# Kernel optimization log

Hardware: AMD Instinct MI355X
Metric: run time of the kernel (lower is better)

Reference implementation:

```python
import jax, jax.numpy as jnp
import numpy as np

DIM = 512
NUM_HEADS = 8


def setup_inputs() -> dict:
    key = jax.random.key(0)
    ks = jax.random.split(key, 10)
    B, N, C = 2, 4096, DIM
    s = 0.02
    return {
        "x": jax.random.normal(ks[0], (B, N, C), dtype=jnp.float32),
        "Wq": jax.random.normal(ks[1], (C, C), dtype=jnp.float32) * s,
        "Wk": jax.random.normal(ks[2], (C, C), dtype=jnp.float32) * s,
        "Wv": jax.random.normal(ks[3], (C, C), dtype=jnp.float32) * s,
        "Wattn": jax.random.normal(ks[4], (C, C), dtype=jnp.float32) * s,
        "Wconv": jax.random.normal(ks[5], (C, C), dtype=jnp.float32) * s,
        "dw_kernel": jax.random.normal(ks[6], (C, 1, 3), dtype=jnp.float32) * s,  # depthwise (O, I/groups, K)
        "dw_bias": jax.random.normal(ks[7], (C,), dtype=jnp.float32) * s,
        "Wcout": jax.random.normal(ks[8], (C, C), dtype=jnp.float32) * s,
        "H": 8,
        "W": 512,
    }


def reference(x, Wq, Wk, Wv, Wattn, Wconv, dw_kernel, dw_bias, Wcout, H, W):
    B, N, C = x.shape
    nh = NUM_HEADS
    hd = C // nh
    scale = hd ** (-0.5)

    # QKV projections (torch Linear: x @ W.T), split heads -> [B, nh, N, hd]
    q = (x @ Wq.T).reshape(B, N, nh, hd).transpose(0, 2, 1, 3)
    k = (x @ Wk.T).reshape(B, N, nh, hd).transpose(0, 2, 1, 3)
    v = (x @ Wv.T).reshape(B, N, nh, hd).transpose(0, 2, 1, 3)

    # Materialized N x N attention (faithful to source)
    scores = jnp.einsum("bhqd,bhkd->bhqk", q, k) * scale
    weights = jax.nn.softmax(scores, axis=-1)
    attn = jnp.einsum("bhqk,bhkd->bhqd", weights, v)
    attn = attn.transpose(0, 2, 1, 3).reshape(B, N, C)
    attn_out = attn @ Wattn.T

    # Parallel depthwise-conv branch
    ci = (x @ Wconv.T).transpose(0, 2, 1)  # [B, C, N]
    co = jax.lax.conv_general_dilated(
        ci, dw_kernel,
        window_strides=(1,), padding=((1, 1),),
        feature_group_count=C,
        dimension_numbers=("NCH", "OIH", "NCH"),
    ) + dw_bias[None, :, None]
    conv_out = co.transpose(0, 2, 1) @ Wcout.T  # [B, N, C]

    out = attn_out + conv_out
    # NOTE: source shadows arg H with num_heads before the view
    return out.reshape(B, nh, W, C)
```

## Files before the change

### kernel.cpp

```cpp
#include <hip/hip_runtime.h>

typedef __attribute__((ext_vector_type(8))) short bf16x8;
typedef __attribute__((ext_vector_type(4))) float f32x4;

constexpr int kB = 2, kN = 4096, kC = 512, kNH = 8, kHD = 64;
constexpr int kBN = kB * kN;
constexpr int kWElems = 262144;
constexpr int kWAll = 6 * kWElems;
constexpr int kWExtra = 3584;
constexpr float kQScale = 0.1803368801f;

__device__ __forceinline__ short f2bf(float f) {
  union { float f; unsigned u; } v; v.f = f;
  unsigned r = v.u + 0x7fffu + ((v.u >> 16) & 1u);
  return (short)(r >> 16);
}
__device__ __forceinline__ float bf2f(short s) {
  union { unsigned u; float f; } v; v.u = ((unsigned)(unsigned short)s) << 16;
  return v.f;
}
__device__ __forceinline__ float exp2_(float x) {
#if __has_builtin(__builtin_amdgcn_exp2f)
  return __builtin_amdgcn_exp2f(x);
#else
  return exp2f(x);
#endif
}
__device__ __forceinline__ unsigned pk2bf(float a, float b) {
  union { float f; unsigned u; } ua, ub; ua.f = a; ub.f = b;
#if __has_builtin(__builtin_amdgcn_perm)
  return __builtin_amdgcn_perm(ub.u + 0x8000u, ua.u + 0x8000u, 0x07060302u);
#else
  return ((ua.u + 0x8000u) >> 16) | (((ub.u + 0x8000u) >> 16) << 16);
#endif
}

__device__ __forceinline__ bf16x8 ld8(const short* p) { return *(const bf16x8*)p; }
__device__ __forceinline__ bf16x8 ld8(const float* p) {
  float4 a = *(const float4*)p;
  float4 b = *(const float4*)(p + 4);
  bf16x8 r;
  r[0] = f2bf(a.x); r[1] = f2bf(a.y); r[2] = f2bf(a.z); r[3] = f2bf(a.w);
  r[4] = f2bf(b.x); r[5] = f2bf(b.y); r[6] = f2bf(b.z); r[7] = f2bf(b.w);
  return r;
}
__device__ __forceinline__ void stf(short* p, float v) { *p = f2bf(v); }
__device__ __forceinline__ void stf(float* p, float v) { *p = v; }

__device__ __forceinline__ void gload_lds16(const void* g, void* l) {
  __builtin_amdgcn_global_load_lds(
      (const __attribute__((address_space(1))) void*)g,
      (__attribute__((address_space(3))) void*)l, 16, 0, 0);
}

__global__ void detect_dtype(const unsigned* __restrict__ x, int* __restrict__ flag) {
  const int lane = threadIdx.x & 63;
  unsigned w = x[lane];
  int e = (int)((w >> 7) & 0xffu);
  bool bf = (e >= 100 && e <= 140);
  unsigned long long m = __ballot(bf);
  if (lane == 0) *flag = (__popcll(m) >= 32) ? 1 : 0;
}

constexpr int kW8 = kWAll / 8;
constexpr int kX8 = kBN * kC / 8;
__global__ __launch_bounds__(256) void convert_all(
    const void* Wq, const void* Wk, const void* Wv, const void* Wc,
    const void* Wa, const void* Wco, const void* dwk, const void* dwb,
    const void* x, const int* __restrict__ flag, short* __restrict__ dst,
    short* __restrict__ xb) {
  const int gtid = blockIdx.x * 256 + threadIdx.x;
  const bool bf = (*flag != 0);
  if (gtid < kW8) {
    const int e = gtid * 8;
    const int t = e >> 18, off = e & (kWElems - 1);
    const void* src = (t == 0) ? Wq : (t == 1) ? Wk : (t == 2) ? Wv
                    : (t == 3) ? Wc : (t == 4) ? Wa : Wco;
    bf16x8 v = bf ? ld8((const short*)src + off) : ld8((const float*)src + off);
    *(bf16x8*)(dst + e) = v;
  } else if (gtid < kW8 + kWExtra) {
    const int eoff = gtid - kW8;
    if (eoff < 1536) {
      dst[kWAll + eoff] = bf ? ((const short*)dwk)[eoff]
                             : f2bf(((const float*)dwk)[eoff]);
    } else if (eoff < 2048) {
      const int i = eoff - 1536;
      dst[kWAll + 1536 + i] = bf ? ((const short*)dwb)[i]
                                 : f2bf(((const float*)dwb)[i]);
    } else {
      const int t2 = eoff - 2048;
      const int tap = t2 >> 9, c = t2 & 511;
      dst[kWAll + 2048 + t2] = bf ? ((const short*)dwk)[c * 3 + tap]
                                  : f2bf(((const float*)dwk)[c * 3 + tap]);
    }
  } else if (gtid < kW8 + kWExtra + kX8) {
    const int e = (gtid - kW8 - kWExtra) * 8;
    bf16x8 v = bf ? ld8((const short*)x + e) : ld8((const float*)x + e);
    *(bf16x8*)(xb + e) = v;
  }
}

__global__ __launch_bounds__(256, 3) void proj_gemm(
    const short* __restrict__ xb, const short* __restrict__ wb,
    short* __restrict__ q, short* __restrict__ k, short* __restrict__ vT,
    short* __restrict__ ci) {
  __shared__ __align__(16) short As[128 * 64];
  __shared__ __align__(16) short Bs[128 * 64];
  const int t = threadIdx.x;
  const int wave = t >> 6, lane = t & 63;
  const int row = lane & 15, quad = lane >> 4;
  const int bn = blockIdx.x & 15;
  const int bm = blockIdx.x >> 4;
  const int m0 = bm * 128, n0 = bn * 128;
  const int wm = wave & 1, wn = wave >> 1;
  const int lrow = lane >> 3, lch = lane & 7;

  f32x4 acc[4][4];
#pragma unroll
  for (int mi = 0; mi < 4; ++mi)
#pragma unroll
    for (int ni = 0; ni < 4; ++ni)
#pragma unroll
      for (int r = 0; r < 4; ++r) acc[mi][ni][r] = 0.0f;

  for (int k0 = 0; k0 < kC; k0 += 64) {
#pragma unroll
    for (int p = 0; p < 4; ++p) {
      const int m = wave * 32 + p * 8 + lrow;
      const int kch = lch ^ (m & 7);
      gload_lds16(xb + (size_t)(m0 + m) * kC + k0 + kch * 8,
                  &As[(wave * 32 + p * 8) * 64]);
      gload_lds16(wb + (size_t)(n0 + m) * kC + k0 + kch * 8,
                  &Bs[(wave * 32 + p * 8) * 64]);
    }
    __syncthreads();

#pragma unroll
    for (int kk2 = 0; kk2 < 2; ++kk2) {
      bf16x8 af[4], bfr[4];
#pragma unroll
      for (int mi = 0; mi < 4; ++mi) {
        const int m = wm * 64 + mi * 16 + row;
        const int ch = (kk2 * 4 + quad) ^ (m & 7);
        af[mi] = *(const bf16x8*)(&As[m * 64 + ch * 8]);
      }
#pragma unroll
      for (int ni = 0; ni < 4; ++ni) {
        const int n = wn * 64 + ni * 16 + row;
        const int ch = (kk2 * 4 + quad) ^ (n & 7);
        bfr[ni] = *(const bf16x8*)(&Bs[n * 64 + ch * 8]);
      }
#pragma unroll
      for (int mi = 0; mi < 4; ++mi)
#pragma unroll
        for (int ni = 0; ni < 4; ++ni)
          acc[mi][ni] = __builtin_amdgcn_mfma_f32_16x16x32_bf16(
              af[mi], bfr[ni], acc[mi][ni], 0, 0, 0);
    }
    __syncthreads();
  }

  const int gc0 = n0 + wn * 64;
  const int mat = gc0 >> 9;
  const float scale = (mat == 0) ? kQScale : 1.0f;
#pragma unroll
  for (int mi = 0; mi < 4; ++mi) {
#pragma unroll
    for (int ni = 0; ni < 4; ++ni) {
#pragma unroll
      for (int r = 0; r < 4; ++r) {
        const int gm = m0 + wm * 64 + mi * 16 + quad * 4 + r;
        const int c_ = ((gc0 + ni * 16) & 511) + row;
        const int b_ = gm >> 12;
        const int n_ = gm & (kN - 1);
        const short bv = f2bf(acc[mi][ni][r] * scale);
        if (mat == 3) {
          ci[(b_ * kN + n_) * kC + c_] = bv;
        } else {
          const int h = c_ >> 6, d = c_ & 63;
          const int bh = b_ * kNH + h;
          if (mat == 0)      q[(bh * kN + n_) * kHD + d] = bv;
          else if (mat == 1) k[(bh * kN + n_) * kHD + d] = bv;
          else               vT[(bh * kHD + d) * kN + n_] = bv;
        }
      }
    }
  }
}

__global__ __launch_bounds__(256) void dwconv(
    const short* __restrict__ ci, const short* __restrict__ wb,
    short* __restrict__ cb) {
  const int e0 = (blockIdx.x * 256 + threadIdx.x) * 8;
  const int c0 = e0 & (kC - 1);
  const int bn = e0 >> 9;
  const int n_ = bn & (kN - 1);
  bf16x8 xc = ld8(ci + e0);
  bf16x8 xm, xp;
  if (n_ > 0) xm = ld8(ci + e0 - kC);
  else
#pragma unroll
    for (int i = 0; i < 8; ++i) xm[i] = 0;
  if (n_ < kN - 1) xp = ld8(ci + e0 + kC);
  else
#pragma unroll
    for (int i = 0; i < 8; ++i) xp[i] = 0;
  bf16x8 w0 = ld8(wb + kWAll + 2048 + c0);
  bf16x8 w1 = ld8(wb + kWAll + 2048 + 512 + c0);
  bf16x8 w2 = ld8(wb + kWAll + 2048 + 1024 + c0);
  bf16x8 bi = ld8(wb + kWAll + 1536 + c0);
  bf16x8 o;
#pragma unroll
  for (int i = 0; i < 8; ++i) {
    float a = bf2f(bi[i]) + bf2f(xm[i]) * bf2f(w0[i]) +
              bf2f(xc[i]) * bf2f(w1[i]) + bf2f(xp[i]) * bf2f(w2[i]);
    o[i] = f2bf(a);
  }
  *(bf16x8*)(cb + e0) = o;
}

__global__ __launch_bounds__(256, 3) void attn_flash(
    const short* __restrict__ q, const short* __restrict__ k,
    const short* __restrict__ vT, short* __restrict__ attn) {
  __shared__ __align__(16) short Kb[2][64 * 72];
  __shared__ __align__(16) short VbS[2][64 * 72];
  const int t = threadIdx.x;
  const int wave = t >> 6;
  const int lane = t & 63;
  const int row = lane & 15;
  const int quad = lane >> 4;

  const int slot = blockIdx.x & 7;
  const int inner = blockIdx.x >> 3;
  const int bh = slot * 2 + (inner & 1);
  const int q0 = (inner >> 1) * 128 + wave * 32;

  const short* qbase = q + (bh * kN + q0) * kHD;
  const short* kbase = k + bh * kN * kHD;
  const short* vbase = vT + bh * kHD * kN;

  bf16x8 qb[2][2];
#pragma unroll
  for (int g = 0; g < 2; ++g) {
    qb[g][0] = *(const bf16x8*)(qbase + (g * 16 + row) * kHD + quad * 8);
    qb[g][1] = *(const bf16x8*)(qbase + (g * 16 + row) * kHD + 32 + quad * 8);
  }

  f32x4 o[2][4];
#pragma unroll
  for (int g = 0; g < 2; ++g)
#pragma unroll
    for (int j = 0; j < 4; ++j)
#pragma unroll
      for (int r = 0; r < 4; ++r) o[g][j][r] = 0.0f;
  float l_[2] = {0.0f, 0.0f};

  const int i0 = t, i1 = t + 256;
  const int sr0 = i0 >> 3, sc0 = i0 & 7;
  const int sr1 = i1 >> 3, sc1 = i1 & 7;
  const int vb0 = (sc0 >> 2) * 32 + (sc0 & 1) * 16 + (sc0 & 2) * 2;
  const int vb1 = (sc1 >> 2) * 32 + (sc1 & 1) * 16 + (sc1 & 2) * 2;

  auto stage_v = [&](int buf, bf16x8 v0, bf16x8 v1) {
    *(short4*)(&VbS[buf][sr0 * 72 + vb0]) =
        make_short4(v0[0], v0[1], v0[2], v0[3]);
    *(short4*)(&VbS[buf][sr0 * 72 + vb0 + 8]) =
        make_short4(v0[4], v0[5], v0[6], v0[7]);
    *(short4*)(&VbS[buf][sr1 * 72 + vb1]) =
        make_short4(v1[0], v1[1], v1[2], v1[3]);
    *(short4*)(&VbS[buf][sr1 * 72 + vb1 + 8]) =
        make_short4(v1[4], v1[5], v1[6], v1[7]);
  };

  {
    bf16x8 ka = *(const bf16x8*)(kbase + i0 * 8);
    bf16x8 kb2 = *(const bf16x8*)(kbase + i1 * 8);
    *(bf16x8*)(&Kb[0][sr0 * 72 + sc0 * 8]) = ka;
    *(bf16x8*)(&Kb[0][sr1 * 72 + sc1 * 8]) = kb2;
    bf16x8 v0 = *(const bf16x8*)(vbase + sr0 * kN + sc0 * 8);
    bf16x8 v1 = *(const bf16x8*)(vbase + sr1 * kN + sc1 * 8);
    stage_v(0, v0, v1);
  }
  __syncthreads();

  for (int kt = 0; kt < kN / 64; ++kt) {
    const int cur = kt & 1;
    const bool more = (kt < kN / 64 - 1);
    bf16x8 kn0, kn1, vn0, vn1;
    if (more) {
      kn0 = *(const bf16x8*)(kbase + (kt + 1) * 4096 + i0 * 8);
      kn1 = *(const bf16x8*)(kbase + (kt + 1) * 4096 + i1 * 8);
      vn0 = *(const bf16x8*)(vbase + sr0 * kN + (kt + 1) * 64 + sc0 * 8);
      vn1 = *(const bf16x8*)(vbase + sr1 * kN + (kt + 1) * 64 + sc1 * 8);
    }

    f32x4 s[2][4];
#pragma unroll
    for (int g = 0; g < 2; ++g)
#pragma unroll
      for (int jk = 0; jk < 4; ++jk)
#pragma unroll
        for (int r = 0; r < 4; ++r) s[g][jk][r] = 0.0f;
#pragma unroll
    for (int jk = 0; jk < 4; ++jk) {
      const short* kr = &Kb[cur][(jk * 16 + row) * 72 + quad * 8];
      bf16x8 a0 = *(const bf16x8*)kr;
      bf16x8 a1 = *(const bf16x8*)(kr + 32);
#pragma unroll
      for (int g = 0; g < 2; ++g) {
        s[g][jk] = __builtin_amdgcn_mfma_f32_16x16x32_bf16(a0, qb[g][0], s[g][jk], 0, 0, 0);
        s[g][jk] = __builtin_amdgcn_mfma_f32_16x16x32_bf16(a1, qb[g][1], s[g][jk], 0, 0, 0);
      }
    }

    bf16x8 pb[2][2];
#pragma unroll
    for (int g = 0; g < 2; ++g) {
      float rs = 0.0f;
#pragma unroll
      for (int jk = 0; jk < 4; ++jk)
#pragma unroll
        for (int r = 0; r < 4; ++r) {
          float p = exp2_(s[g][jk][r]);
          s[g][jk][r] = p;
          rs += p;
        }
      l_[g] += rs;
#pragma unroll
      for (int c = 0; c < 2; ++c) {
        union { unsigned u[4]; bf16x8 v; } pu;
        pu.u[0] = pk2bf(s[g][2 * c][0], s[g][2 * c][1]);
        pu.u[1] = pk2bf(s[g][2 * c][2], s[g][2 * c][3]);
        pu.u[2] = pk2bf(s[g][2 * c + 1][0], s[g][2 * c + 1][1]);
        pu.u[3] = pk2bf(s[g][2 * c + 1][2], s[g][2 * c + 1][3]);
        pb[g][c] = pu.v;
      }
    }

#pragma unroll
    for (int jd = 0; jd < 4; ++jd) {
      const short* vb = &VbS[cur][(jd * 16 + row) * 72 + quad * 8];
#pragma unroll
      for (int c = 0; c < 2; ++c) {
        bf16x8 av = *(const bf16x8*)(vb + c * 32);
#pragma unroll
        for (int g = 0; g < 2; ++g)
          o[g][jd] = __builtin_amdgcn_mfma_f32_16x16x32_bf16(
              av, pb[g][c], o[g][jd], 0, 0, 0);
      }
    }

    if (more) {
      *(bf16x8*)(&Kb[1 - cur][sr0 * 72 + sc0 * 8]) = kn0;
      *(bf16x8*)(&Kb[1 - cur][sr1 * 72 + sc1 * 8]) = kn1;
      stage_v(1 - cur, vn0, vn1);
    }
    __syncthreads();
  }

  const int b_ = bh >> 3, h = bh & 7;
#pragma unroll
  for (int g = 0; g < 2; ++g) {
    float lt = l_[g];
    lt += __shfl_xor(lt, 16);
    lt += __shfl_xor(lt, 32);
    const float linv = 1.0f / lt;
    const int n_ = q0 + g * 16 + row;
    short* ob = attn + (b_ * kN + n_) * kC + h * kHD + quad * 4;
#pragma unroll
    for (int jd = 0; jd < 4; ++jd) {
      short4 st = make_short4(f2bf(o[g][jd][0] * linv), f2bf(o[g][jd][1] * linv),
                              f2bf(o[g][jd][2] * linv), f2bf(o[g][jd][3] * linv));
      *(short4*)(ob + jd * 16) = st;
    }
  }
}

template <typename TO>
__device__ __forceinline__ void out_body(
    const short* __restrict__ attn, const short* __restrict__ cb,
    const short* __restrict__ wb, TO* __restrict__ out) {
  __shared__ __align__(16) short As[128 * 64];
  __shared__ __align__(16) short Bs[64 * 64];
  const int t = threadIdx.x;
  const int wave = t >> 6, lane = t & 63;
  const int row = lane & 15, quad = lane >> 4;
  const int bn = blockIdx.x & 7;
  const int bm = blockIdx.x >> 3;
  const int m0 = bm * 128, n0 = bn * 64;
  const int wm = wave & 1, wn = wave >> 1;
  const int lrow = lane >> 3, lch = lane & 7;

  f32x4 acc[4][2];
#pragma unroll
  for (int mi = 0; mi < 4; ++mi)
#pragma unroll
    for (int ni = 0; ni < 2; ++ni)
#pragma unroll
      for (int r = 0; r < 4; ++r) acc[mi][ni][r] = 0.0f;

  const short* Wa = wb + 4 * kWElems;
  const short* Wo = wb + 5 * kWElems;

  for (int k0 = 0; k0 < 1024; k0 += 64) {
    const short* Asrc = (k0 < 512) ? attn : cb;
    const short* Bsrc = (k0 < 512) ? Wa : Wo;
    const int ka = k0 & 511;
#pragma unroll
    for (int p = 0; p < 4; ++p) {
      const int m = wave * 32 + p * 8 + lrow;
      const int kch = lch ^ (m & 7);
      gload_lds16(Asrc + (size_t)(m0 + m) * kC + ka + kch * 8,
                  &As[(wave * 32 + p * 8) * 64]);
    }
#pragma unroll
    for (int p = 0; p < 2; ++p) {
      const int n = wave * 16 + p * 8 + lrow;
      const int kch = lch ^ (n & 7);
      gload_lds16(Bsrc + (size_t)(n0 + n) * kC + ka + kch * 8,
                  &Bs[(wave * 16 + p * 8) * 64]);
    }
    __syncthreads();

#pragma unroll
    for (int kk2 = 0; kk2 < 2; ++kk2) {
      bf16x8 af[4], bfr[2];
#pragma unroll
      for (int mi = 0; mi < 4; ++mi) {
        const int m = wm * 64 + mi * 16 + row;
        const int ch = (kk2 * 4 + quad) ^ (m & 7);
        af[mi] = *(const bf16x8*)(&As[m * 64 + ch * 8]);
      }
#pragma unroll
      for (int ni = 0; ni < 2; ++ni) {
        const int n = wn * 32 + ni * 16 + row;
        const int ch = (kk2 * 4 + quad) ^ (n & 7);
        bfr[ni] = *(const bf16x8*)(&Bs[n * 64 + ch * 8]);
      }
#pragma unroll
      for (int mi = 0; mi < 4; ++mi)
#pragma unroll
        for (int ni = 0; ni < 2; ++ni)
          acc[mi][ni] = __builtin_amdgcn_mfma_f32_16x16x32_bf16(
              af[mi], bfr[ni], acc[mi][ni], 0, 0, 0);
    }
    __syncthreads();
  }

#pragma unroll
  for (int mi = 0; mi < 4; ++mi)
#pragma unroll
    for (int ni = 0; ni < 2; ++ni)
#pragma unroll
      for (int r = 0; r < 4; ++r) {
        const int gm = m0 + wm * 64 + mi * 16 + quad * 4 + r;
        const int gc = n0 + wn * 32 + ni * 16 + row;
        stf(out + (size_t)gm * kC + gc, acc[mi][ni][r]);
      }
}

__global__ __launch_bounds__(256, 4) void out_gemm(
    const short* __restrict__ attn, const short* __restrict__ cb,
    const short* __restrict__ wb, const int* __restrict__ flag, void* out) {
  if (*flag)
    out_body<short>(attn, cb, wb, (short*)out);
  else
    out_body<float>(attn, cb, wb, (float*)out);
}

extern "C" void kernel_launch(void* const* d_in, const int* in_sizes, int n_in,
                              void* d_out, int out_size, void* d_ws, size_t ws_size,
                              hipStream_t stream) {
  const void* x   = d_in[0];
  const void* Wq  = d_in[1];
  const void* Wk  = d_in[2];
  const void* Wv  = d_in[3];
  const void* Wa  = d_in[4];
  const void* Wc  = d_in[5];
  const void* dwk = d_in[6];
  const void* dwb = d_in[7];
  const void* Wco = d_in[8];

  short* ws = (short*)d_ws;
  const size_t E = (size_t)kBN * kC;
  int*   flag = (int*)ws;
  short* wb   = ws + 256;
  short* q    = wb + kWAll + kWExtra;
  short* k    = q + E;
  short* vT   = k + E;
  short* ci   = vT + E;
  short* cb   = ci + E;
  short* attn = ci;
  short* xb   = cb;

  detect_dtype<<<1, 64, 0, stream>>>((const unsigned*)x, flag);
  const int cvt_threads = kW8 + kWExtra + kX8;
  convert_all<<<(cvt_threads + 255) / 256, 256, 0, stream>>>(
      Wq, Wk, Wv, Wc, Wa, Wco, dwk, dwb, x, flag, wb, xb);
  proj_gemm<<<1024, 256, 0, stream>>>(xb, wb, q, k, vT, ci);
  dwconv<<<(kBN * kC) / (256 * 8), 256, 0, stream>>>(ci, wb, cb);
  attn_flash<<<512, 256, 0, stream>>>(q, k, vT, attn);
  out_gemm<<<512, 256, 0, stream>>>(attn, cb, wb, flag, d_out);
}
```

Measured before the change: 246.0 us.

## Halve attention query tile per block and double grid for occupancy

Each wave in the flash attention kernel now processes 16 query rows instead of 32, so a block covers 64 queries and the grid doubles to 1024 blocks. Launch bounds move from 3 to 4 blocks per SIMD budget. This cuts register pressure and raises the number of resident waves to hide latency. The cost is half the reuse of each staged K/V tile, which doubles K/V global and LDS traffic per query.

```diff
diff --git a/kernel.cpp b/kernel.cpp
--- a/kernel.cpp
+++ b/kernel.cpp
@@ -219,7 +219,7 @@
   *(bf16x8*)(cb + e0) = o;
 }
 
-__global__ __launch_bounds__(256, 3) void attn_flash(
+__global__ __launch_bounds__(256, 4) void attn_flash(
     const short* __restrict__ q, const short* __restrict__ k,
     const short* __restrict__ vT, short* __restrict__ attn) {
   __shared__ __align__(16) short Kb[2][64 * 72];
@@ -233,27 +233,22 @@
   const int slot = blockIdx.x & 7;
   const int inner = blockIdx.x >> 3;
   const int bh = slot * 2 + (inner & 1);
-  const int q0 = (inner >> 1) * 128 + wave * 32;
-
-  const short* qbase = q + (bh * kN + q0) * kHD;
-  const short* kbase = k + bh * kN * kHD;
-  const short* vbase = vT + bh * kHD * kN;
-
-  bf16x8 qb[2][2];
-#pragma unroll
-  for (int g = 0; g < 2; ++g) {
-    qb[g][0] = *(const bf16x8*)(qbase + (g * 16 + row) * kHD + quad * 8);
-    qb[g][1] = *(const bf16x8*)(qbase + (g * 16 + row) * kHD + 32 + quad * 8);
-  }
-
-  f32x4 o[2][4];
-#pragma unroll
-  for (int g = 0; g < 2; ++g)
-#pragma unroll
-    for (int j = 0; j < 4; ++j)
-#pragma unroll
-      for (int r = 0; r < 4; ++r) o[g][j][r] = 0.0f;
-  float l_[2] = {0.0f, 0.0f};
+  const int q0 = (inner >> 1) * 64 + wave * 16;
+
+  const short* qbase = q + (size_t)(bh * kN + q0) * kHD;
+  const short* kbase = k + (size_t)bh * kN * kHD;
+  const short* vbase = vT + (size_t)bh * kHD * kN;
+
+  bf16x8 qb[2];
+  qb[0] = *(const bf16x8*)(qbase + row * kHD + quad * 8);
+  qb[1] = *(const bf16x8*)(qbase + row * kHD + 32 + quad * 8);
+
+  f32x4 o[4];
+#pragma unroll
+  for (int jd = 0; jd < 4; ++jd)
+#pragma unroll
+    for (int r = 0; r < 4; ++r) o[jd][r] = 0.0f;
+  float l_ = 0.0f;
 
   const int i0 = t, i1 = t + 256;
   const int sr0 = i0 >> 3, sc0 = i0 & 7;
@@ -294,47 +289,39 @@
       vn1 = *(const bf16x8*)(vbase + sr1 * kN + (kt + 1) * 64 + sc1 * 8);
     }
 
-    f32x4 s[2][4];
-#pragma unroll
-    for (int g = 0; g < 2; ++g)
-#pragma unroll
-      for (int jk = 0; jk < 4; ++jk)
-#pragma unroll
-        for (int r = 0; r < 4; ++r) s[g][jk][r] = 0.0f;
+    f32x4 s[4];
+#pragma unroll
+    for (int jk = 0; jk < 4; ++jk)
+#pragma unroll
+      for (int r = 0; r < 4; ++r) s[jk][r] = 0.0f;
 #pragma unroll
     for (int jk = 0; jk < 4; ++jk) {
       const short* kr = &Kb[cur][(jk * 16 + row) * 72 + quad * 8];
       bf16x8 a0 = *(const bf16x8*)kr;
       bf16x8 a1 = *(const bf16x8*)(kr + 32);
-#pragma unroll
-      for (int g = 0; g < 2; ++g) {
-        s[g][jk] = __builtin_amdgcn_mfma_f32_16x16x32_bf16(a0, qb[g][0], s[g][jk], 0, 0, 0);
-        s[g][jk] = __builtin_amdgcn_mfma_f32_16x16x32_bf16(a1, qb[g][1], s[g][jk], 0, 0, 0);
-      }
-    }
-
-    bf16x8 pb[2][2];
-#pragma unroll
-    for (int g = 0; g < 2; ++g) {
-      float rs = 0.0f;
-#pragma unroll
-      for (int jk = 0; jk < 4; ++jk)
-#pragma unroll
-        for (int r = 0; r < 4; ++r) {
-          float p = exp2_(s[g][jk][r]);
-          s[g][jk][r] = p;
-          rs += p;
-        }
-      l_[g] += rs;
-#pragma unroll
-      for (int c = 0; c < 2; ++c) {
-        union { unsigned u[4]; bf16x8 v; } pu;
-        pu.u[0] = pk2bf(s[g][2 * c][0], s[g][2 * c][1]);
-        pu.u[1] = pk2bf(s[g][2 * c][2], s[g][2 * c][3]);
-        pu.u[2] = pk2bf(s[g][2 * c + 1][0], s[g][2 * c + 1][1]);
-        pu.u[3] = pk2bf(s[g][2 * c + 1][2], s[g][2 * c + 1][3]);
-        pb[g][c] = pu.v;
-      }
+      s[jk] = __builtin_amdgcn_mfma_f32_16x16x32_bf16(a0, qb[0], s[jk], 0, 0, 0);
+      s[jk] = __builtin_amdgcn_mfma_f32_16x16x32_bf16(a1, qb[1], s[jk], 0, 0, 0);
+    }
+
+    float rs = 0.0f;
+#pragma unroll
+    for (int jk = 0; jk < 4; ++jk)
+#pragma unroll
+      for (int r = 0; r < 4; ++r) {
+        float p = exp2_(s[jk][r]);
+        s[jk][r] = p;
+        rs += p;
+      }
+    l_ += rs;
+    bf16x8 pb[2];
+#pragma unroll
+    for (int c = 0; c < 2; ++c) {
+      union { unsigned u[4]; bf16x8 v; } pu;
+      pu.u[0] = pk2bf(s[2 * c][0], s[2 * c][1]);
+      pu.u[1] = pk2bf(s[2 * c][2], s[2 * c][3]);
+      pu.u[2] = pk2bf(s[2 * c + 1][0], s[2 * c + 1][1]);
+      pu.u[3] = pk2bf(s[2 * c + 1][2], s[2 * c + 1][3]);
+      pb[c] = pu.v;
     }
 
 #pragma unroll
@@ -343,10 +330,7 @@
 #pragma unroll
       for (int c = 0; c < 2; ++c) {
         bf16x8 av = *(const bf16x8*)(vb + c * 32);
-#pragma unroll
-        for (int g = 0; g < 2; ++g)
-          o[g][jd] = __builtin_amdgcn_mfma_f32_16x16x32_bf16(
-              av, pb[g][c], o[g][jd], 0, 0, 0);
+        o[jd] = __builtin_amdgcn_mfma_f32_16x16x32_bf16(av, pb[c], o[jd], 0, 0, 0);
       }
     }
 
@@ -359,20 +343,17 @@
   }
 
   const int b_ = bh >> 3, h = bh & 7;
-#pragma unroll
-  for (int g = 0; g < 2; ++g) {
-    float lt = l_[g];
-    lt += __shfl_xor(lt, 16);
-    lt += __shfl_xor(lt, 32);
-    const float linv = 1.0f / lt;
-    const int n_ = q0 + g * 16 + row;
-    short* ob = attn + (b_ * kN + n_) * kC + h * kHD + quad * 4;
-#pragma unroll
-    for (int jd = 0; jd < 4; ++jd) {
-      short4 st = make_short4(f2bf(o[g][jd][0] * linv), f2bf(o[g][jd][1] * linv),
-                              f2bf(o[g][jd][2] * linv), f2bf(o[g][jd][3] * linv));
-      *(short4*)(ob + jd * 16) = st;
-    }
+  float lt = l_;
+  lt += __shfl_xor(lt, 16);
+  lt += __shfl_xor(lt, 32);
+  const float linv = 1.0f / lt;
+  const int n_ = q0 + row;
+  short* ob = attn + (size_t)(b_ * kN + n_) * kC + h * kHD + quad * 4;
+#pragma unroll
+  for (int jd = 0; jd < 4; ++jd) {
+    short4 st = make_short4(f2bf(o[jd][0] * linv), f2bf(o[jd][1] * linv),
+                            f2bf(o[jd][2] * linv), f2bf(o[jd][3] * linv));
+    *(short4*)(ob + jd * 16) = st;
   }
 }
 
@@ -499,6 +480,6 @@
       Wq, Wk, Wv, Wc, Wa, Wco, dwk, dwb, x, flag, wb, xb);
   proj_gemm<<<1024, 256, 0, stream>>>(xb, wb, q, k, vT, ci);
   dwconv<<<(kBN * kC) / (256 * 8), 256, 0, stream>>>(ci, wb, cb);
-  attn_flash<<<512, 256, 0, stream>>>(q, k, vT, attn);
+  attn_flash<<<1024, 256, 0, stream>>>(q, k, vT, attn);
   out_gemm<<<512, 256, 0, stream>>>(attn, cb, wb, flag, d_out);
 }
```

Measured after the change: 275.3 us. 1.12x slower.

## Restructure flash attention K/V pipeline with direct-to-LDS swizzled loads and two-tile phases

Applied to the files above, without the earlier changes.

The attention kernel now processes two 64-key tiles per barrier phase. K is loaded straight into LDS through gload_lds16 into an XOR-swizzled unpadded layout, and V for the next phase is staged between the two tile computations. The aim is to halve the number of barriers and overlap global loads with MFMA work, with s_setprio raised around the MFMA sections. In exchange, LDS use doubles and launch bounds drop from 3 to 2 blocks per CU, which lowers occupancy.

```diff
diff --git a/kernel.cpp b/kernel.cpp
--- a/kernel.cpp
+++ b/kernel.cpp
@@ -219,11 +219,11 @@
   *(bf16x8*)(cb + e0) = o;
 }
 
-__global__ __launch_bounds__(256, 3) void attn_flash(
+__global__ __launch_bounds__(256, 2) void attn_flash(
     const short* __restrict__ q, const short* __restrict__ k,
     const short* __restrict__ vT, short* __restrict__ attn) {
-  __shared__ __align__(16) short Kb[2][64 * 72];
-  __shared__ __align__(16) short VbS[2][64 * 72];
+  __shared__ __align__(16) short Kb[2][2][64 * 64];
+  __shared__ __align__(16) short VbS[2][2][64 * 72];
   const int t = threadIdx.x;
   const int wave = t >> 6;
   const int lane = t & 63;
@@ -235,9 +235,9 @@
   const int bh = slot * 2 + (inner & 1);
   const int q0 = (inner >> 1) * 128 + wave * 32;
 
-  const short* qbase = q + (bh * kN + q0) * kHD;
-  const short* kbase = k + bh * kN * kHD;
-  const short* vbase = vT + bh * kHD * kN;
+  const short* qbase = q + (size_t)(bh * kN + q0) * kHD;
+  const short* kbase = k + (size_t)bh * kN * kHD;
+  const short* vbase = vT + (size_t)bh * kHD * kN;
 
   bf16x8 qb[2][2];
 #pragma unroll
@@ -254,6 +254,9 @@
 #pragma unroll
       for (int r = 0; r < 4; ++r) o[g][j][r] = 0.0f;
   float l_[2] = {0.0f, 0.0f};
+
+  const int ksrow = lane >> 3;
+  const int kschunk = (lane & 7) ^ ksrow;
 
   const int i0 = t, i1 = t + 256;
   const int sr0 = i0 >> 3, sc0 = i0 & 7;
@@ -261,39 +264,31 @@
   const int vb0 = (sc0 >> 2) * 32 + (sc0 & 1) * 16 + (sc0 & 2) * 2;
   const int vb1 = (sc1 >> 2) * 32 + (sc1 & 1) * 16 + (sc1 & 2) * 2;
 
-  auto stage_v = [&](int buf, bf16x8 v0, bf16x8 v1) {
-    *(short4*)(&VbS[buf][sr0 * 72 + vb0]) =
+  auto stage_v = [&](int ph, int tl, bf16x8 v0, bf16x8 v1) {
+    *(short4*)(&VbS[ph][tl][sr0 * 72 + vb0]) =
         make_short4(v0[0], v0[1], v0[2], v0[3]);
-    *(short4*)(&VbS[buf][sr0 * 72 + vb0 + 8]) =
+    *(short4*)(&VbS[ph][tl][sr0 * 72 + vb0 + 8]) =
         make_short4(v0[4], v0[5], v0[6], v0[7]);
-    *(short4*)(&VbS[buf][sr1 * 72 + vb1]) =
+    *(short4*)(&VbS[ph][tl][sr1 * 72 + vb1]) =
         make_short4(v1[0], v1[1], v1[2], v1[3]);
-    *(short4*)(&VbS[buf][sr1 * 72 + vb1 + 8]) =
+    *(short4*)(&VbS[ph][tl][sr1 * 72 + vb1 + 8]) =
         make_short4(v1[4], v1[5], v1[6], v1[7]);
   };
-
-  {
-    bf16x8 ka = *(const bf16x8*)(kbase + i0 * 8);
-    bf16x8 kb2 = *(const bf16x8*)(kbase + i1 * 8);
-    *(bf16x8*)(&Kb[0][sr0 * 72 + sc0 * 8]) = ka;
-    *(bf16x8*)(&Kb[0][sr1 * 72 + sc1 * 8]) = kb2;
-    bf16x8 v0 = *(const bf16x8*)(vbase + sr0 * kN + sc0 * 8);
-    bf16x8 v1 = *(const bf16x8*)(vbase + sr1 * kN + sc1 * 8);
-    stage_v(0, v0, v1);
-  }
-  __syncthreads();
-
-  for (int kt = 0; kt < kN / 64; ++kt) {
-    const int cur = kt & 1;
-    const bool more = (kt < kN / 64 - 1);
-    bf16x8 kn0, kn1, vn0, vn1;
-    if (more) {
-      kn0 = *(const bf16x8*)(kbase + (kt + 1) * 4096 + i0 * 8);
-      kn1 = *(const bf16x8*)(kbase + (kt + 1) * 4096 + i1 * 8);
-      vn0 = *(const bf16x8*)(vbase + sr0 * kN + (kt + 1) * 64 + sc0 * 8);
-      vn1 = *(const bf16x8*)(vbase + sr1 * kN + (kt + 1) * 64 + sc1 * 8);
-    }
-
+  auto stage_k = [&](int ph, int kt2) {
+#pragma unroll
+    for (int tl = 0; tl < 2; ++tl)
+#pragma unroll
+      for (int j = 0; j < 2; ++j)
+        gload_lds16(
+            kbase + (size_t)((kt2 + tl) * 64 + j * 32 + wave * 8 + ksrow) * 64 +
+                kschunk * 8,
+            &Kb[ph][tl][j * 2048 + wave * 512]);
+  };
+
+  const int c0s = ((quad) ^ (row & 7)) * 8;
+  const int c1s = ((quad + 4) ^ (row & 7)) * 8;
+
+  auto tile_step = [&](const short* kt_base, const short* vt_base) {
     f32x4 s[2][4];
 #pragma unroll
     for (int g = 0; g < 2; ++g)
@@ -301,31 +296,31 @@
       for (int jk = 0; jk < 4; ++jk)
 #pragma unroll
         for (int r = 0; r < 4; ++r) s[g][jk][r] = 0.0f;
+    __builtin_amdgcn_s_setprio(1);
 #pragma unroll
     for (int jk = 0; jk < 4; ++jk) {
-      const short* kr = &Kb[cur][(jk * 16 + row) * 72 + quad * 8];
-      bf16x8 a0 = *(const bf16x8*)kr;
-      bf16x8 a1 = *(const bf16x8*)(kr + 32);
+      const short* kr = kt_base + (jk * 16 + row) * 64;
+      bf16x8 a0 = *(const bf16x8*)(kr + c0s);
+      bf16x8 a1 = *(const bf16x8*)(kr + c1s);
 #pragma unroll
       for (int g = 0; g < 2; ++g) {
         s[g][jk] = __builtin_amdgcn_mfma_f32_16x16x32_bf16(a0, qb[g][0], s[g][jk], 0, 0, 0);
         s[g][jk] = __builtin_amdgcn_mfma_f32_16x16x32_bf16(a1, qb[g][1], s[g][jk], 0, 0, 0);
       }
     }
+    __builtin_amdgcn_s_setprio(0);
 
     bf16x8 pb[2][2];
 #pragma unroll
     for (int g = 0; g < 2; ++g) {
-      float rs = 0.0f;
-#pragma unroll
-      for (int jk = 0; jk < 4; ++jk)
-#pragma unroll
-        for (int r = 0; r < 4; ++r) {
-          float p = exp2_(s[g][jk][r]);
-          s[g][jk][r] = p;
-          rs += p;
-        }
-      l_[g] += rs;
+      float tj[4];
+#pragma unroll
+      for (int jk = 0; jk < 4; ++jk) {
+#pragma unroll
+        for (int r = 0; r < 4; ++r) s[g][jk][r] = exp2_(s[g][jk][r]);
+        tj[jk] = (s[g][jk][0] + s[g][jk][1]) + (s[g][jk][2] + s[g][jk][3]);
+      }
+      l_[g] += (tj[0] + tj[1]) + (tj[2] + tj[3]);
 #pragma unroll
       for (int c = 0; c < 2; ++c) {
         union { unsigned u[4]; bf16x8 v; } pu;
@@ -337,9 +332,10 @@
       }
     }
 
+    __builtin_amdgcn_s_setprio(1);
 #pragma unroll
     for (int jd = 0; jd < 4; ++jd) {
-      const short* vb = &VbS[cur][(jd * 16 + row) * 72 + quad * 8];
+      const short* vb = vt_base + (jd * 16 + row) * 72 + quad * 8;
 #pragma unroll
       for (int c = 0; c < 2; ++c) {
         bf16x8 av = *(const bf16x8*)(vb + c * 32);
@@ -349,12 +345,41 @@
               av, pb[g][c], o[g][jd], 0, 0, 0);
       }
     }
-
+    __builtin_amdgcn_s_setprio(0);
+  };
+
+  {
+    stage_k(0, 0);
+    bf16x8 a = *(const bf16x8*)(vbase + sr0 * kN + sc0 * 8);
+    bf16x8 b = *(const bf16x8*)(vbase + sr1 * kN + sc1 * 8);
+    stage_v(0, 0, a, b);
+    a = *(const bf16x8*)(vbase + sr0 * kN + 64 + sc0 * 8);
+    b = *(const bf16x8*)(vbase + sr1 * kN + 64 + sc1 * 8);
+    stage_v(0, 1, a, b);
+  }
+  __syncthreads();
+
+  for (int p = 0; p < 32; ++p) {
+    const int cur = p & 1;
+    const bool more = (p < 31);
+    bf16x8 vn00, vn01, vn10, vn11;
     if (more) {
-      *(bf16x8*)(&Kb[1 - cur][sr0 * 72 + sc0 * 8]) = kn0;
-      *(bf16x8*)(&Kb[1 - cur][sr1 * 72 + sc1 * 8]) = kn1;
-      stage_v(1 - cur, vn0, vn1);
-    }
+      const int kk = (2 * p + 2) * 64;
+      stage_k(1 - cur, 2 * p + 2);
+      vn00 = *(const bf16x8*)(vbase + sr0 * kN + kk + sc0 * 8);
+      vn01 = *(const bf16x8*)(vbase + sr1 * kN + kk + sc1 * 8);
+      vn10 = *(const bf16x8*)(vbase + sr0 * kN + kk + 64 + sc0 * 8);
+      vn11 = *(const bf16x8*)(vbase + sr1 * kN + kk + 64 + sc1 * 8);
+    }
+
+    tile_step(&Kb[cur][0][0], &VbS[cur][0][0]);
+
+    if (more) {
+      stage_v(1 - cur, 0, vn00, vn01);
+      stage_v(1 - cur, 1, vn10, vn11);
+    }
+
+    tile_step(&Kb[cur][1][0], &VbS[cur][1][0]);
     __syncthreads();
   }
 
@@ -366,7 +391,7 @@
     lt += __shfl_xor(lt, 32);
     const float linv = 1.0f / lt;
     const int n_ = q0 + g * 16 + row;
-    short* ob = attn + (b_ * kN + n_) * kC + h * kHD + quad * 4;
+    short* ob = attn + (size_t)(b_ * kN + n_) * kC + h * kHD + quad * 4;
 #pragma unroll
     for (int jd = 0; jd < 4; ++jd) {
       short4 st = make_short4(f2bf(o[g][jd][0] * linv), f2bf(o[g][jd][1] * linv),
```

Measured after the change: 259.2 us. +5.4%, slower.
